# Performance work log

Measured on AMD Instinct MI355X. Metric: run time of the kernel, lower is better.

## Reference

```python
import jax, jax.numpy as jnp
import numpy as np

VAR_NUM = [29, 2, 1, 6, 7, 59, 1, 24, 76, 711, 3, 9, 1]  # sums to 929
TEMP = 0.8
EPS = 1e-20


def setup_inputs() -> dict:
    key = jax.random.key(0)
    ks = jax.random.split(key, 8)
    B, D, H, O = 32768, 128, 1024, 929
    s = lambda n: 1.0 / np.sqrt(n)
    return {
        "x": jax.random.normal(ks[0], (B, D), jnp.float32),
        "W1": jax.random.uniform(ks[1], (D, H), jnp.float32, -s(D), s(D)),
        "b1": jax.random.uniform(ks[2], (H,), jnp.float32, -s(D), s(D)),
        "W2": jax.random.uniform(ks[3], (H, H), jnp.float32, -s(H), s(H)),
        "b2": jax.random.uniform(ks[4], (H,), jnp.float32, -s(H), s(H)),
        "W3": jax.random.uniform(ks[5], (H, O), jnp.float32, -s(H), s(H)),
        "b3": jax.random.uniform(ks[6], (O,), jnp.float32, -s(H), s(H)),
        "u": jax.random.uniform(ks[7], (B, O), jnp.float32),  # U(0,1) gumbel base noise
    }


def reference(x, W1, b1, W2, b2, W3, b3, u):
    h = jax.nn.elu(x @ W1 + b1)          # [B, H]
    h = jax.nn.sigmoid(h @ W2 + b2)      # [B, H]
    logits = h @ W3 + b3                 # [B, 929]
    g = -jnp.log(-jnp.log(u + EPS) + EPS)  # gumbel noise, [B, 929]
    outs = []
    off = 0
    for n in VAR_NUM:  # fixed 13 segments
        seg = logits[:, off:off + n]
        if n == 1:
            outs.append(seg)  # passthrough for continuous columns
        else:
            y = (seg + g[:, off:off + n]) / TEMP
            outs.append(jax.nn.softmax(y, axis=-1))
        off += n
    return jnp.concatenate(outs, axis=1)  # [B, 929]
```

## Files before the change

### kernel.cpp

```cpp
#include <hip/hip_runtime.h>
#include <hip/hip_bf16.h>
#include <stdint.h>

#define GEPS 1e-20f

typedef __bf16 bf16x8 __attribute__((ext_vector_type(8)));
typedef float  f32x4  __attribute__((ext_vector_type(4)));

typedef const __attribute__((address_space(1))) uint32_t* gptr32;
typedef __attribute__((address_space(3))) uint32_t* lptr32;

__device__ __forceinline__ void load_lds16(const void* g, void* l) {
    __builtin_amdgcn_global_load_lds((gptr32)g, (lptr32)l, 16, 0, 0);
}

__device__ __forceinline__ uint16_t f2bf(float v) {
    __hip_bfloat16 b = __float2bfloat16(v);
    return *(uint16_t*)&b;
}
__device__ __forceinline__ float bf2f(uint16_t b) {
    uint32_t u = (uint32_t)b << 16;
    return __builtin_bit_cast(float, u);
}

#define LN2   0.69314718056f
#define LOG2E 1.44269504089f
__device__ __forceinline__ float fast_log(float x) { return __builtin_amdgcn_logf(x) * LN2; }
__device__ __forceinline__ float fast_exp(float x) { return __builtin_amdgcn_exp2f(x * LOG2E); }
__device__ __forceinline__ float fast_exp2(float x) { return __builtin_amdgcn_exp2f(x); }
__device__ __forceinline__ float fast_rcp(float x)  { return __builtin_amdgcn_rcpf(x); }

__device__ __forceinline__ void store_val(uint16_t* C, size_t idx, float v) { C[idx] = f2bf(v); }
__device__ __forceinline__ void store_val(float* C, size_t idx, float v)    { C[idx] = v; }

__global__ void cast_bf16(const float* __restrict__ in, uint16_t* __restrict__ out, int n) {
    int i = (blockIdx.x * blockDim.x + threadIdx.x) * 4;
    if (i < n) {
        float4 v = *(const float4*)(in + i);
        ushort4 o;
        o.x = f2bf(v.x); o.y = f2bf(v.y); o.z = f2bf(v.z); o.w = f2bf(v.w);
        *(ushort4*)(out + i) = o;
    }
}

__global__ void transpose_cast(const float* __restrict__ W, uint16_t* __restrict__ Wt,
                               int K, int N, int Npad) {
    __shared__ float tile[64][65];
    const int k0 = blockIdx.y * 64, n0 = blockIdx.x * 64;
    const int tx = threadIdx.x & 63, ty = threadIdx.x >> 6;
    for (int r = ty; r < 64; r += 4) {
        int n = n0 + tx;
        tile[r][tx] = (n < N) ? W[(size_t)(k0 + r) * N + n] : 0.f;
    }
    __syncthreads();
    for (int r = ty; r < 64; r += 4) {
        Wt[(size_t)(n0 + r) * K + k0 + tx] = f2bf(tile[tx][r]);
    }
}

template<int ACT, typename OutT, bool SNG>
__global__ __launch_bounds__(256)
void gemm_bt(const uint16_t* __restrict__ A, const uint16_t* __restrict__ Bt,
             const float* __restrict__ bias, OutT* __restrict__ C,
             float* __restrict__ sngl,
             int K, int Nout, int ldc) {
    __shared__ __align__(16) uint16_t As[128 * 32];
    __shared__ __align__(16) uint16_t Bs[128 * 32];

    const int t    = threadIdx.x;
    const int wave = t >> 6, lane = t & 63;

    const int nbx = gridDim.x;
    const int bid = blockIdx.y * nbx + blockIdx.x;
    const int xcd = bid & 7;
    const int s   = bid >> 3;
    const int nidx = s % nbx;
    const int midx = xcd * (gridDim.y >> 3) + s / nbx;

    const int m0 = midx * 128, n0 = nidx * 128;
    const int wm = (wave >> 1) * 64, wn = (wave & 1) * 64;
    const int quad = lane >> 4;
    const int qk   = quad * 8;
    const int r15  = lane & 15;

    f32x4 acc[4][4] = {};

    const uint16_t* Ag = A  + (size_t)m0 * K;
    const uint16_t* Bg = Bt + (size_t)n0 * K;

    for (int k0 = 0; k0 < K; k0 += 32) {
        __syncthreads();
        #pragma unroll
        for (int rd = 0; rd < 2; ++rd) {
            int c = t + rd * 256;
            int row = c >> 2, kc = (c & 3) * 8;
            load_lds16(Ag + (size_t)row * K + k0 + kc, &As[c * 8]);
            load_lds16(Bg + (size_t)row * K + k0 + kc, &Bs[c * 8]);
        }
        __syncthreads();

        bf16x8 a[4], b[4];
        #pragma unroll
        for (int i = 0; i < 4; ++i)
            a[i] = *(const bf16x8*)&As[(wm + i * 16 + r15) * 32 + qk];
        #pragma unroll
        for (int i = 0; i < 4; ++i)
            b[i] = *(const bf16x8*)&Bs[(wn + i * 16 + r15) * 32 + qk];

        #pragma unroll
        for (int mi = 0; mi < 4; ++mi)
            #pragma unroll
            for (int ni = 0; ni < 4; ++ni)
                acc[mi][ni] = __builtin_amdgcn_mfma_f32_16x16x32_bf16(
                    a[mi], b[ni], acc[mi][ni], 0, 0, 0);
    }

    #pragma unroll
    for (int ni = 0; ni < 4; ++ni) {
        int col = n0 + wn + ni * 16 + r15;
        if (col < Nout) {
            float bv = bias[col];
            bool is_sng = SNG && (col == 31 || col == 104 || col == 928);
            #pragma unroll
            for (int mi = 0; mi < 4; ++mi) {
                #pragma unroll
                for (int r = 0; r < 4; ++r) {
                    int row = m0 + wm + mi * 16 + quad * 4 + r;
                    float v = acc[mi][ni][r] + bv;
                    if (ACT == 1) v = (v > 0.f) ? v : (fast_exp(v) - 1.f);
                    else if (ACT == 2) v = fast_rcp(1.f + fast_exp(-v));
                    store_val(C, (size_t)row * ldc + col, v);
                    if constexpr (SNG) {
                        if (is_sng) sngl[(size_t)row * 929 + col] = v;
                    }
                }
            }
        }
    }
}

#define BARRIER() asm volatile("s_barrier" ::: "memory")
#define LGKM0()   asm volatile("s_waitcnt lgkmcnt(0)" ::: "memory")
#define VMW8()    asm volatile("s_waitcnt vmcnt(8)" ::: "memory")
#define VMW0()    asm volatile("s_waitcnt vmcnt(0)" ::: "memory")
#define PRIO1()   __builtin_amdgcn_s_setprio(1)
#define PRIO0()   __builtin_amdgcn_s_setprio(0)

template<int ACT, typename OutT, bool SNG, int K>
__global__ __launch_bounds__(512, 2)
void gemm256(const uint16_t* __restrict__ A, const uint16_t* __restrict__ Bt,
             const float* __restrict__ bias, OutT* __restrict__ C,
             float* __restrict__ sngl, int Nout, int ldc) {
    constexpr int NT = K / 64;
    constexpr int NI = NT / 2;
    constexpr int KB = K * 2;
    __shared__ __align__(16) char lds[131072];
    constexpr int AOFF0 = 0, BOFF0 = 32768, AOFF1 = 65536, BOFF1 = 98304;

    const int t = threadIdx.x;
    const int wave = t >> 6, lane = t & 63;
    const int quad = lane >> 4, r15 = lane & 15;
    const int wm = (wave >> 2) * 128, wn = (wave & 3) * 64;

    const int nbx = gridDim.x;
    const int bid = blockIdx.y * nbx + blockIdx.x;
    const int xcd = bid & 7;
    const int sb  = bid >> 3;
    const int nidx = sb % nbx;
    const int midx = xcd * (gridDim.y >> 3) + sb / nbx;
    const int m0 = midx * 256, n0 = nidx * 256;

    const int srow = t >> 3;
    const int scb  = ((t & 7) ^ (srow & 7)) << 4;
    const char* Asrc = (const char*)A  + (size_t)(m0 + srow) * KB + scb;
    const char* Bsrc = (const char*)Bt + (size_t)(n0 + srow) * KB + scb;

    const int sx   = (r15 & 7) << 4;
    const int cb0  = (quad * 16) ^ sx;
    const int cb1  = (64 + quad * 16) ^ sx;
    const int aRow = (wm + r15) * 128;
    const int bRow = (wn + r15) * 128;

    f32x4 acc[8][4] = {};
    bf16x8 a[4][2], b[4][2];

#define STG(src, half, tile, ldsOff)                                                      \
    do {                                                                                  \
        const char* _s = (src) + (size_t)((half) * 128) * KB + (size_t)(tile) * 128;      \
        load_lds16(_s,                   &lds[(ldsOff) + (half) * 16384 + t * 16]);       \
        load_lds16(_s + (size_t)64 * KB, &lds[(ldsOff) + (half) * 16384 + 8192 + t * 16]);\
    } while (0)

    auto ldA = [&](int buf, int mh) {
        #pragma unroll
        for (int mi = 0; mi < 4; ++mi) {
            const int base = buf * 65536 + aRow + (mh * 4 + mi) * 2048;
            a[mi][0] = *(const bf16x8*)&lds[base + cb0];
            a[mi][1] = *(const bf16x8*)&lds[base + cb1];
        }
    };
    auto ldB = [&](int buf, int nh) {
        #pragma unroll
        for (int ni = 0; ni < 2; ++ni) {
            const int base = buf * 65536 + 32768 + bRow + (nh * 2 + ni) * 2048;
            b[nh * 2 + ni][0] = *(const bf16x8*)&lds[base + cb0];
            b[nh * 2 + ni][1] = *(const bf16x8*)&lds[base + cb1];
        }
    };
    auto mfmaQ = [&](int mlo, int nlo) {
        #pragma unroll
        for (int mi = 0; mi < 4; ++mi)
            #pragma unroll
            for (int ni = 0; ni < 2; ++ni)
                #pragma unroll
                for (int kk = 0; kk < 2; ++kk)
                    acc[mlo + mi][nlo + ni] = __builtin_amdgcn_mfma_f32_16x16x32_bf16(
                        a[mi][kk], b[nlo + ni][kk], acc[mlo + mi][nlo + ni], 0, 0, 0);
    };

    STG(Bsrc, 0, 0, BOFF0); STG(Bsrc, 1, 0, BOFF0);
    STG(Asrc, 0, 0, AOFF0); STG(Asrc, 1, 0, AOFF0);
    STG(Bsrc, 0, 1, BOFF1); STG(Bsrc, 1, 1, BOFF1);
    STG(Asrc, 0, 1, AOFF1); STG(Asrc, 1, 1, AOFF1);
    VMW8(); BARRIER();

    #pragma unroll 1
    for (int ki = 0; ki < NI; ++ki) {
        const int p0 = (2 * ki + 2) & (NT - 1);
        const int p1 = (2 * ki + 3) & (NT - 1);

        ldA(0, 0); ldB(0, 0);
        BARRIER();
        PRIO1(); mfmaQ(0, 0); PRIO0();
        LGKM0(); BARRIER();

        ldB(0, 1);
        BARRIER();
        PRIO1(); mfmaQ(0, 2); PRIO0();
        LGKM0(); BARRIER();

        ldA(0, 1);
        STG(Bsrc, 0, p0, BOFF0); STG(Bsrc, 1, p0, BOFF0);
        BARRIER();
        PRIO1(); mfmaQ(4, 2); PRIO0();
        LGKM0(); BARRIER();

        STG(Asrc, 0, p0, AOFF0); STG(Asrc, 1, p0, AOFF0);
        BARRIER();
        PRIO1(); mfmaQ(4, 0); PRIO0();
        VMW8(); BARRIER();

        ldA(1, 0); ldB(1, 0);
        BARRIER();
        PRIO1(); mfmaQ(0, 0); PRIO0();
        LGKM0(); BARRIER();

        ldB(1, 1);
        BARRIER();
        PRIO1(); mfmaQ(0, 2); PRIO0();
        LGKM0(); BARRIER();

        ldA(1, 1);
        STG(Bsrc, 0, p1, BOFF1); STG(Bsrc, 1, p1, BOFF1);
        BARRIER();
        PRIO1(); mfmaQ(4, 2); PRIO0();
        LGKM0(); BARRIER();

        STG(Asrc, 0, p1, AOFF1); STG(Asrc, 1, p1, AOFF1);
        BARRIER();
        PRIO1(); mfmaQ(4, 0); PRIO0();
        VMW8(); BARRIER();
    }
    VMW0();
    BARRIER();

#undef STG

    #pragma unroll
    for (int ni = 0; ni < 4; ++ni) {
        const int col = wn + ni * 16 + r15;
        const int gc  = n0 + col;
        const float bv = (gc < Nout) ? bias[gc] : 0.f;
        const bool is_sng = SNG && (gc == 31 || gc == 104 || gc == 928);
        #pragma unroll
        for (int mi = 0; mi < 8; ++mi) {
            #pragma unroll
            for (int r = 0; r < 4; ++r) {
                const int row = wm + mi * 16 + quad * 4 + r;
                float v = acc[mi][ni][r] + bv;
                if (ACT == 1) v = (v > 0.f) ? v : (fast_exp(v) - 1.f);
                else if (ACT == 2) v = fast_rcp(1.f + fast_exp(-v));
                *(uint16_t*)&lds[row * 512 + ((col * 2) ^ ((row & 7) << 4))] = f2bf(v);
                if constexpr (SNG) {
                    if (is_sng) sngl[(size_t)(m0 + row) * 929 + gc] = v;
                }
            }
        }
    }
    LGKM0(); BARRIER();

    {
        const int rt = t >> 5;
        const int cc = t & 31;
        #pragma unroll 1
        for (int pass = 0; pass < 16; ++pass) {
            const int row = pass * 16 + rt;
            f32x4 v4 = *(const f32x4*)&lds[row * 512 + ((cc * 16) ^ ((row & 7) << 4))];
            *(f32x4*)&C[(size_t)(m0 + row) * ldc + n0 + cc * 8] = v4;
        }
    }
}

#define NEG_BIG (-1e30f)
#define Y2_LG   1.8033688011f

__device__ __forceinline__ float y2_col(const uint16_t* __restrict__ rlg,
                                        const float* __restrict__ ru, int c) {
    float l2u   = __builtin_amdgcn_logf(ru[c] + GEPS);
    float inner = fmaf(-LN2, l2u, GEPS);
    float l2i   = __builtin_amdgcn_logf(inner);
    return fmaf(Y2_LG, bf2f(rlg[c]), -1.25f * l2i);
}

template<int N, int OFF>
__device__ __forceinline__ void seg_small(const uint16_t* __restrict__ rlg,
                                          const float* __restrict__ ru,
                                          float* __restrict__ rout, int l32) {
    static_assert(N <= 32, "seg_small needs N<=32");
    constexpr int GS = (N <= 2) ? 2 : (N <= 4) ? 4 : (N <= 8) ? 8 : (N <= 16) ? 16 : 32;
    const bool act = l32 < N;
    const int  c   = OFF + l32;
    float y = act ? y2_col(rlg, ru, c) : NEG_BIG;
    float m = y;
    #pragma unroll
    for (int o = 1; o < GS; o <<= 1) m = fmaxf(m, __shfl_xor(m, o, 64));
    float e = act ? fast_exp2(y - m) : 0.f;
    float s = e;
    #pragma unroll
    for (int o = 1; o < GS; o <<= 1) s += __shfl_xor(s, o, 64);
    if (act) rout[c] = e * fast_rcp(s);
}

template<int N, int OFF>
__device__ __forceinline__ void seg_wide(const uint16_t* __restrict__ rlg,
                                         const float* __restrict__ ru,
                                         float* __restrict__ rout, int lane) {
    constexpr int IT = (N + 63) / 64;
    float y[IT];
    float m = NEG_BIG;
    #pragma unroll
    for (int i = 0; i < IT; ++i) {
        const int j = i * 64 + lane;
        y[i] = (j < N) ? y2_col(rlg, ru, OFF + j) : NEG_BIG;
        m = fmaxf(m, y[i]);
    }
    #pragma unroll
    for (int o = 1; o < 64; o <<= 1) m = fmaxf(m, __shfl_xor(m, o, 64));
    float s = 0.f;
    #pragma unroll
    for (int i = 0; i < IT; ++i) {
        float e = fast_exp2(y[i] - m);
        y[i] = e;
        s += e;
    }
    #pragma unroll
    for (int o = 1; o < 64; o <<= 1) s += __shfl_xor(s, o, 64);
    const float inv = fast_rcp(s);
    #pragma unroll
    for (int i = 0; i < IT; ++i) {
        const int j = i * 64 + lane;
        if (j < N) rout[OFF + j] = y[i] * inv;
    }
}

__global__ __launch_bounds__(256)
void gumbel_epilogue(const uint16_t* __restrict__ lg, float* __restrict__ out,
                     const float* __restrict__ u, int B) {
    const int wave = threadIdx.x >> 6, lane = threadIdx.x & 63;
    const int l32  = lane & 31, half = lane >> 5;
    const int rowA = blockIdx.x * 8 + wave * 2;
    if (rowA >= B) return;

    const size_t uoA  = (size_t)rowA * 929;
    const size_t uoB  = uoA + 929;
    const size_t lgoA = (size_t)rowA * 1024;
    const size_t lgoB = lgoA + 1024;
    const size_t uoH  = half ? uoB  : uoA;
    const size_t lgoH = half ? lgoB : lgoA;

    const uint16_t* lgH = lg  + lgoH;
    const float*    uH  = u   + uoH;
    float*          oH  = out + uoH;
    seg_small<29,   0>(lgH, uH, oH, l32);
    seg_small< 2,  29>(lgH, uH, oH, l32);
    seg_small< 6,  32>(lgH, uH, oH, l32);
    seg_small< 7,  38>(lgH, uH, oH, l32);
    seg_small<24, 105>(lgH, uH, oH, l32);
    seg_small< 3, 916>(lgH, uH, oH, l32);
    seg_small< 9, 919>(lgH, uH, oH, l32);

    const uint16_t* lgA = lg + lgoA; const float* uA = u + uoA; float* oA = out + uoA;
    const uint16_t* lgB = lg + lgoB; const float* uB = u + uoB; float* oB = out + uoB;
    seg_wide< 59,  45>(lgA, uA, oA, lane);
    seg_wide< 59,  45>(lgB, uB, oB, lane);
    seg_wide< 76, 129>(lgA, uA, oA, lane);
    seg_wide< 76, 129>(lgB, uB, oB, lane);
    seg_wide<711, 205>(lgA, uA, oA, lane);
    seg_wide<711, 205>(lgB, uB, oB, lane);
}

extern "C" void kernel_launch(void* const* d_in, const int* in_sizes, int n_in,
                              void* d_out, int out_size, void* d_ws, size_t ws_size,
                              hipStream_t stream) {
    const float* x  = (const float*)d_in[0];
    const float* W1 = (const float*)d_in[1];
    const float* b1 = (const float*)d_in[2];
    const float* W2 = (const float*)d_in[3];
    const float* b2 = (const float*)d_in[4];
    const float* W3 = (const float*)d_in[5];
    const float* b3 = (const float*)d_in[6];
    const float* u  = (const float*)d_in[7];
    float* out = (float*)d_out;

    const int B = 32768, D = 128, H = 1024, O = 929, OP = 1024;

    char* ws = (char*)d_ws;
    uint16_t* xb  = (uint16_t*)ws; ws += (size_t)B * D * 2;
    uint16_t* w1t = (uint16_t*)ws; ws += (size_t)H * D * 2;
    uint16_t* w2t = (uint16_t*)ws; ws += (size_t)H * H * 2;
    uint16_t* w3t = (uint16_t*)ws; ws += (size_t)OP * H * 2;
    uint16_t* h1  = (uint16_t*)ws; ws += (size_t)B * H * 2;
    uint16_t* h2  = (uint16_t*)ws; ws += (size_t)B * H * 2;
    uint16_t* lg  = h1;

    cast_bf16<<<(B * D / 4 + 255) / 256, 256, 0, stream>>>(x, xb, B * D);
    transpose_cast<<<dim3(H / 64, D / 64), 256, 0, stream>>>(W1, w1t, D, H, H);
    transpose_cast<<<dim3(H / 64, H / 64), 256, 0, stream>>>(W2, w2t, H, H, H);
    transpose_cast<<<dim3(OP / 64, H / 64), 256, 0, stream>>>(W3, w3t, H, O, OP);

    gemm_bt<1, uint16_t, false><<<dim3(H / 128, B / 128), 256, 0, stream>>>(
        xb, w1t, b1, h1, nullptr, D, H, H);
    gemm256<2, uint16_t, false, 1024><<<dim3(H / 256, B / 256), 512, 0, stream>>>(
        h1, w2t, b2, h2, nullptr, H, H);
    gemm256<0, uint16_t, true, 1024><<<dim3(OP / 256, B / 256), 512, 0, stream>>>(
        h2, w3t, b3, lg, out, O, 1024);

    gumbel_epilogue<<<B / 8, 256, 0, stream>>>(lg, out, u, B);
}
```

Baseline: 463.7 us.

## Restructure gemm256 mainloop into 4-stage K=32 ring with register double-buffering

Replaces the 2-stage K=64 LDS double buffer with a 4-slot ring of K=32 tiles, giving a deeper prefetch. LDS reads for the next quarter are issued into separate register sets (aLo/aHi, bE/bO) while MFMAs run on the current ones. The explicit lgkmcnt waits and the extra barriers between sub-steps are removed, and the swizzle is changed for 64-byte rows. This aims to overlap global loads, LDS reads and MFMA more fully and to cut barrier stalls. It relies on compiler-inserted lgkm waits and on vmcnt(6) accounting being correct, so there is a risk of races or stalls.

```diff
diff --git a/kernel.cpp b/kernel.cpp
--- a/kernel.cpp
+++ b/kernel.cpp
@@ -140,9 +140,9 @@
 }
 
 #define BARRIER() asm volatile("s_barrier" ::: "memory")
-#define LGKM0()   asm volatile("s_waitcnt lgkmcnt(0)" ::: "memory")
+#define VMW6()    asm volatile("s_waitcnt vmcnt(6)" ::: "memory")
 #define VMW8()    asm volatile("s_waitcnt vmcnt(8)" ::: "memory")
-#define VMW0()    asm volatile("s_waitcnt vmcnt(0)" ::: "memory")
+#define DRAIN()   asm volatile("s_waitcnt vmcnt(0) lgkmcnt(0)" ::: "memory")
 #define PRIO1()   __builtin_amdgcn_s_setprio(1)
 #define PRIO0()   __builtin_amdgcn_s_setprio(0)
 
@@ -151,11 +151,11 @@
 void gemm256(const uint16_t* __restrict__ A, const uint16_t* __restrict__ Bt,
              const float* __restrict__ bias, OutT* __restrict__ C,
              float* __restrict__ sngl, int Nout, int ldc) {
-    constexpr int NT = K / 64;
-    constexpr int NI = NT / 2;
+    constexpr int NT = K / 32;
+    constexpr int NI = NT / 4;
     constexpr int KB = K * 2;
+    static_assert(NT >= 8 && (NT & (NT - 1)) == 0, "need pow2 >= 8 tiles");
     __shared__ __align__(16) char lds[131072];
-    constexpr int AOFF0 = 0, BOFF0 = 32768, AOFF1 = 65536, BOFF1 = 98304;
 
     const int t = threadIdx.x;
     const int wave = t >> 6, lane = t & 63;
@@ -170,111 +170,87 @@
     const int midx = xcd * (gridDim.y >> 3) + sb / nbx;
     const int m0 = midx * 256, n0 = nidx * 256;
 
-    const int srow = t >> 3;
-    const int scb  = ((t & 7) ^ (srow & 7)) << 4;
-    const char* Asrc = (const char*)A  + (size_t)(m0 + srow) * KB + scb;
-    const char* Bsrc = (const char*)Bt + (size_t)(n0 + srow) * KB + scb;
-
-    const int sx   = (r15 & 7) << 4;
-    const int cb0  = (quad * 16) ^ sx;
-    const int cb1  = (64 + quad * 16) ^ sx;
-    const int aRow = (wm + r15) * 128;
-    const int bRow = (wn + r15) * 128;
+    const int scb = ((t & 3) ^ ((t >> 3) & 3)) << 4;
+    const char* Asrc = (const char*)A  + (size_t)(m0 + (t >> 2)) * KB + scb;
+    const char* Bsrc = (const char*)Bt + (size_t)(n0 + (t >> 2)) * KB + scb;
+
+    const int cbR   = (quad ^ ((r15 >> 1) & 3)) << 4;
+    const int aRowB = (wm + r15) * 64;
+    const int bRowB = (wn + r15) * 64;
 
     f32x4 acc[8][4] = {};
-    bf16x8 a[4][2], b[4][2];
-
-#define STG(src, half, tile, ldsOff)                                                      \
-    do {                                                                                  \
-        const char* _s = (src) + (size_t)((half) * 128) * KB + (size_t)(tile) * 128;      \
-        load_lds16(_s,                   &lds[(ldsOff) + (half) * 16384 + t * 16]);       \
-        load_lds16(_s + (size_t)64 * KB, &lds[(ldsOff) + (half) * 16384 + 8192 + t * 16]);\
-    } while (0)
-
-    auto ldA = [&](int buf, int mh) {
-        #pragma unroll
-        for (int mi = 0; mi < 4; ++mi) {
-            const int base = buf * 65536 + aRow + (mh * 4 + mi) * 2048;
-            a[mi][0] = *(const bf16x8*)&lds[base + cb0];
-            a[mi][1] = *(const bf16x8*)&lds[base + cb1];
-        }
-    };
-    auto ldB = [&](int buf, int nh) {
-        #pragma unroll
-        for (int ni = 0; ni < 2; ++ni) {
-            const int base = buf * 65536 + 32768 + bRow + (nh * 2 + ni) * 2048;
-            b[nh * 2 + ni][0] = *(const bf16x8*)&lds[base + cb0];
-            b[nh * 2 + ni][1] = *(const bf16x8*)&lds[base + cb1];
-        }
-    };
-    auto mfmaQ = [&](int mlo, int nlo) {
+    bf16x8 aLo[4], aHi[4], bE[4], bO[4];
+
+    auto stgA = [&](int buf, int tile) {
+        const char* s = Asrc + tile * 64;
+        load_lds16(s,                    &lds[buf * 32768 + t * 16]);
+        load_lds16(s + (size_t)128 * KB, &lds[buf * 32768 + 8192 + t * 16]);
+    };
+    auto stgB = [&](int buf, int tile) {
+        const char* s = Bsrc + tile * 64;
+        load_lds16(s,                    &lds[buf * 32768 + 16384 + t * 16]);
+        load_lds16(s + (size_t)128 * KB, &lds[buf * 32768 + 24576 + t * 16]);
+    };
+    auto rdAlo = [&](int buf) {
+        #pragma unroll
+        for (int i = 0; i < 4; ++i)
+            aLo[i] = *(const bf16x8*)&lds[buf * 32768 + aRowB + i * 1024 + cbR];
+    };
+    auto rdAhi = [&](int buf) {
+        #pragma unroll
+        for (int i = 0; i < 4; ++i)
+            aHi[i] = *(const bf16x8*)&lds[buf * 32768 + aRowB + (4 + i) * 1024 + cbR];
+    };
+    auto rdB = [&](int buf, bf16x8 (&b)[4]) {
+        #pragma unroll
+        for (int i = 0; i < 4; ++i)
+            b[i] = *(const bf16x8*)&lds[buf * 32768 + 16384 + bRowB + i * 1024 + cbR];
+    };
+    auto mfma16 = [&](int mlo, bf16x8 (&a)[4], bf16x8 (&b)[4]) {
         #pragma unroll
         for (int mi = 0; mi < 4; ++mi)
             #pragma unroll
-            for (int ni = 0; ni < 2; ++ni)
-                #pragma unroll
-                for (int kk = 0; kk < 2; ++kk)
-                    acc[mlo + mi][nlo + ni] = __builtin_amdgcn_mfma_f32_16x16x32_bf16(
-                        a[mi][kk], b[nlo + ni][kk], acc[mlo + mi][nlo + ni], 0, 0, 0);
-    };
-
-    STG(Bsrc, 0, 0, BOFF0); STG(Bsrc, 1, 0, BOFF0);
-    STG(Asrc, 0, 0, AOFF0); STG(Asrc, 1, 0, AOFF0);
-    STG(Bsrc, 0, 1, BOFF1); STG(Bsrc, 1, 1, BOFF1);
-    STG(Asrc, 0, 1, AOFF1); STG(Asrc, 1, 1, AOFF1);
+            for (int ni = 0; ni < 4; ++ni)
+                acc[mlo + mi][ni] = __builtin_amdgcn_mfma_f32_16x16x32_bf16(
+                    a[mi], b[ni], acc[mlo + mi][ni], 0, 0, 0);
+    };
+
+    stgA(0, 0); stgB(0, 0);
+    stgA(1, 1); stgB(1, 1);
+    stgA(2, 2); stgB(2, 2);
     VMW8(); BARRIER();
+    rdAlo(0); rdB(0, bE);
 
     #pragma unroll 1
     for (int ki = 0; ki < NI; ++ki) {
-        const int p0 = (2 * ki + 2) & (NT - 1);
-        const int p1 = (2 * ki + 3) & (NT - 1);
-
-        ldA(0, 0); ldB(0, 0);
+        const int T = ki * 4;
+        rdAhi(0); stgA(3, (T + 3) & (NT - 1));
+        PRIO1(); mfma16(0, aLo, bE); PRIO0();
+        VMW6(); BARRIER();
+        rdAlo(1); rdB(1, bO); stgB(3, (T + 3) & (NT - 1));
+        PRIO1(); mfma16(4, aHi, bE); PRIO0();
         BARRIER();
-        PRIO1(); mfmaQ(0, 0); PRIO0();
-        LGKM0(); BARRIER();
-
-        ldB(0, 1);
+        rdAhi(1); stgA(0, (T + 4) & (NT - 1));
+        PRIO1(); mfma16(0, aLo, bO); PRIO0();
+        VMW6(); BARRIER();
+        rdAlo(2); rdB(2, bE); stgB(0, (T + 4) & (NT - 1));
+        PRIO1(); mfma16(4, aHi, bO); PRIO0();
         BARRIER();
-        PRIO1(); mfmaQ(0, 2); PRIO0();
-        LGKM0(); BARRIER();
-
-        ldA(0, 1);
-        STG(Bsrc, 0, p0, BOFF0); STG(Bsrc, 1, p0, BOFF0);
+        rdAhi(2); stgA(1, (T + 5) & (NT - 1));
+        PRIO1(); mfma16(0, aLo, bE); PRIO0();
+        VMW6(); BARRIER();
+        rdAlo(3); rdB(3, bO); stgB(1, (T + 5) & (NT - 1));
+        PRIO1(); mfma16(4, aHi, bE); PRIO0();
         BARRIER();
-        PRIO1(); mfmaQ(4, 2); PRIO0();
-        LGKM0(); BARRIER();
-
-        STG(Asrc, 0, p0, AOFF0); STG(Asrc, 1, p0, AOFF0);
+        rdAhi(3); stgA(2, (T + 6) & (NT - 1));
+        PRIO1(); mfma16(0, aLo, bO); PRIO0();
+        VMW6(); BARRIER();
+        rdAlo(0); rdB(0, bE); stgB(2, (T + 6) & (NT - 1));
+        PRIO1(); mfma16(4, aHi, bO); PRIO0();
         BARRIER();
-        PRIO1(); mfmaQ(4, 0); PRIO0();
-        VMW8(); BARRIER();
-
-        ldA(1, 0); ldB(1, 0);
-        BARRIER();
-        PRIO1(); mfmaQ(0, 0); PRIO0();
-        LGKM0(); BARRIER();
-
-        ldB(1, 1);
-        BARRIER();
-        PRIO1(); mfmaQ(0, 2); PRIO0();
-        LGKM0(); BARRIER();
-
-        ldA(1, 1);
-        STG(Bsrc, 0, p1, BOFF1); STG(Bsrc, 1, p1, BOFF1);
-        BARRIER();
-        PRIO1(); mfmaQ(4, 2); PRIO0();
-        LGKM0(); BARRIER();
-
-        STG(Asrc, 0, p1, AOFF1); STG(Asrc, 1, p1, AOFF1);
-        BARRIER();
-        PRIO1(); mfmaQ(4, 0); PRIO0();
-        VMW8(); BARRIER();
-    }
-    VMW0();
+    }
+    DRAIN();
     BARRIER();
-
-#undef STG
 
     #pragma unroll
     for (int ni = 0; ni < 4; ++ni) {
@@ -297,7 +273,8 @@
             }
         }
     }
-    LGKM0(); BARRIER();
+    asm volatile("s_waitcnt lgkmcnt(0)" ::: "memory");
+    BARRIER();
 
     {
         const int rt = t >> 5;
```

Measured after the change: 465.2 us. No clear change (+0.3%).
